# Optimization experiments

Hardware: AMD Instinct MI355X
Metric: run time of the kernel (lower is better)

Reference implementation:

```python
import jax, jax.numpy as jnp
import numpy as np

B, C, H, W = 4, 64, 128, 128
O = 64
K, S, P, D = 3, 1, 1, 1
K2 = K * K
Ho = (H + 2 * P - D * (K - 1) - 1) // S + 1
Wo = (W + 2 * P - D * (K - 1) - 1) // S + 1


def setup_inputs() -> dict:
    key = jax.random.key(0)
    k1, k2, k3, k4, k5 = jax.random.split(key, 5)
    x = jax.random.normal(k1, (B, C, H, W), dtype=jnp.float32)
    fan = C * K2
    # offset conv: out_channels = 2*n_offsets*K*K = 18; small init so offsets are ~O(1) px
    offset_w = jax.random.normal(k2, (2 * K2, C, K, K), dtype=jnp.float32) * (0.1 / np.sqrt(fan))
    offset_b = jax.random.normal(k3, (2 * K2,), dtype=jnp.float32) * 0.01
    deform_w = jax.random.normal(k4, (O, C, K, K), dtype=jnp.float32) * (1.0 / np.sqrt(fan))
    deform_b = jax.random.normal(k5, (O,), dtype=jnp.float32) * 0.01
    return {"x": x, "offset_w": offset_w, "offset_b": offset_b,
            "deform_w": deform_w, "deform_b": deform_b}


def _conv2d(x, w, b):
    y = jax.lax.conv_general_dilated(
        x, w, window_strides=(S, S), padding=[(P, P), (P, P)],
        rhs_dilation=(D, D), dimension_numbers=("NCHW", "OIHW", "NCHW"))
    return y + b[None, :, None, None]


def _gather(flat, iy, ix, h, w):
    # flat: [B, C, H*W]; iy/ix: [B, K2, Ho, Wo] int32
    valid = (iy >= 0) & (iy < h) & (ix >= 0) & (ix < w)
    idx = jnp.clip(iy, 0, h - 1) * w + jnp.clip(ix, 0, w - 1)
    b = flat.shape[0]
    v = jax.vmap(lambda f, i: f[:, i])(flat, idx.reshape(b, -1))  # [B, C, K2*Ho*Wo]
    v = v.reshape(b, flat.shape[1], *idx.shape[1:])               # [B, C, K2, Ho, Wo]
    return v * valid[:, None].astype(flat.dtype)


def _deform_conv(x, offset, w, b):
    # offset: [B, 2*K2, Ho, Wo] laid out as (dy, dx) pairs per kernel tap (torchvision order)
    off = offset.reshape(B, K2, 2, Ho, Wo)
    dy, dx = off[:, :, 0], off[:, :, 1]                           # [B, K2, Ho, Wo]
    ky = (jnp.arange(K2) // K * D).astype(jnp.float32)
    kx = (jnp.arange(K2) % K * D).astype(jnp.float32)
    base_y = (jnp.arange(Ho) * S - P).astype(jnp.float32)
    base_x = (jnp.arange(Wo) * S - P).astype(jnp.float32)
    py = dy + base_y[None, None, :, None] + ky[None, :, None, None]
    px = dx + base_x[None, None, None, :] + kx[None, :, None, None]

    y0 = jnp.floor(py); x0 = jnp.floor(px)
    wy = py - y0; wx = px - x0
    y0i = y0.astype(jnp.int32); x0i = x0.astype(jnp.int32)
    flat = x.reshape(B, C, H * W)
    w00 = ((1 - wy) * (1 - wx))[:, None]
    w01 = ((1 - wy) * wx)[:, None]
    w10 = (wy * (1 - wx))[:, None]
    w11 = (wy * wx)[:, None]
    sampled = (_gather(flat, y0i, x0i, H, W) * w00
               + _gather(flat, y0i, x0i + 1, H, W) * w01
               + _gather(flat, y0i + 1, x0i, H, W) * w10
               + _gather(flat, y0i + 1, x0i + 1, H, W) * w11)  # [B, C, K2, Ho, Wo]
    out = jnp.einsum("bckhw,ock->bohw", sampled, w.reshape(O, C, K2))
    return out + b[None, :, None, None]


def reference(x, offset_w, offset_b, deform_w, deform_b):
    offset = _conv2d(x, offset_w, offset_b)
    return _deform_conv(x, offset, deform_w, deform_b)
```

## Files before the change

### kernel.cpp

```cpp
#include <hip/hip_runtime.h>

#define BB 4
#define CC 64
#define HH 128
#define WW 128
#define OO 64
#define HWs (HH*WW)

typedef _Float16 f16;
typedef _Float16 f16x8 __attribute__((ext_vector_type(8)));
typedef _Float16 f16x2 __attribute__((ext_vector_type(2)));
typedef float f32x4 __attribute__((ext_vector_type(4)));

__device__ __forceinline__ size_t xt_idx(int b, int y, int x) {
    return (((size_t)b * HH + y) * WW + x) * CC;
}

__global__ __launch_bounds__(256) void prep_all(const float* __restrict__ x,
                                                const float* __restrict__ offw,
                                                const float* __restrict__ dw,
                                                f16* __restrict__ xt,
                                                f16* __restrict__ wA_off,
                                                f16* __restrict__ wA_def) {
    const int bid = blockIdx.x;
    const int tid = threadIdx.x;
    if (bid < 512) {
        const int b = bid >> 7, y = bid & 127;
        const int px = tid & 127, half = tid >> 7;
        const float* src = x + (size_t)b * CC * HWs + (size_t)half * 32 * HWs + y * WW + px;
        f16* dst = xt + xt_idx(b, y, px) + half * 32;
        #pragma unroll
        for (int cg = 0; cg < 4; ++cg) {
            f16x8 v;
            #pragma unroll
            for (int j = 0; j < 8; ++j)
                v[j] = (f16)src[(size_t)(cg * 8 + j) * HWs];
            *(f16x8*)(dst + cg * 8) = v;
        }
    } else {
        const int t = (bid - 512) * 256 + tid;
        const int l = t & 63;
        const int idx = t >> 6;
        f16x8 v;
        if (idx < 36) {
            const int mt = idx & 1, ks = idx >> 1;
            const int o = mt * 16 + (l & 15);
            const int tap = ks >> 1, ky = tap / 3, kx = tap % 3;
            #pragma unroll
            for (int i = 0; i < 8; ++i) {
                const int c = (ks & 1) * 32 + (l >> 4) * 8 + i;
                v[i] = (o < 18) ? (f16)offw[((o * CC + c) * 3 + ky) * 3 + kx] : (f16)0.f;
            }
            *(f16x8*)(wA_off + (size_t)(idx * 64 + l) * 8) = v;
        } else if (idx < 108) {
            const int id2 = idx - 36;
            const int mt = id2 & 3, ks = (id2 >> 2) & 1, tap = id2 >> 3;
            const int o = mt * 16 + (l & 15);
            #pragma unroll
            for (int i = 0; i < 8; ++i) {
                const int c = ks * 32 + (l >> 4) * 8 + i;
                v[i] = (f16)dw[(size_t)(o * CC + c) * 9 + tap];
            }
            *(f16x8*)(wA_def + (size_t)(id2 * 64 + l) * 8) = v;
        }
    }
}

__device__ __forceinline__ f16x8 combine4(f16x8 p00, f16x8 p01, f16x8 p10, f16x8 p11,
                                          f16 h00, f16 h01, f16 h10, f16 h11) {
    const f16x8 W00 = {h00,h00,h00,h00,h00,h00,h00,h00};
    const f16x8 W01 = {h01,h01,h01,h01,h01,h01,h01,h01};
    const f16x8 W10 = {h10,h10,h10,h10,h10,h10,h10,h10};
    const f16x8 W11 = {h11,h11,h11,h11,h11,h11,h11,h11};
    return p00 * W00 + p01 * W01 + p10 * W10 + p11 * W11;
}

__global__ __launch_bounds__(128, 3) void deform_mfma(
    const f16* __restrict__ xt,
    const f16* __restrict__ wA_off,
    const float* __restrict__ offb,
    const f16* __restrict__ wA_def,
    const float* __restrict__ dbias,
    float* __restrict__ out)
{
    __shared__ __align__(16) char win[5 * 36 * 8 * 16];
    __shared__ float offs[18][32];

    const int tid = threadIdx.x;
    const int bid0 = blockIdx.x;
    const int bid = (bid0 & 7) * 256 + (bid0 >> 3);
    const int b = bid >> 9, row = (bid >> 2) & 127, px0 = (bid & 3) * 32;
    const int w = tid >> 6, l = tid & 63;
    const int pxs = l & 15, pxl = w * 16 + pxs, gpx = px0 + pxl, cg = l >> 4;

    #pragma unroll
    for (int it = 0; it < 12; ++it) {
        const int i = tid + it * 128;
        if (i < 5 * 36 * 8) {
            const int s = i / 288, rem = i - s * 288;
            const int xw = rem >> 3, ch8 = rem & 7;
            const int gy = row - 2 + s, gx = px0 - 2 + xw;
            f16x8 v = {};
            if (gy >= 0 && gy < HH && gx >= 0 && gx < WW)
                v = *(const f16x8*)(xt + xt_idx(b, gy, gx) + ch8 * 8);
            *(f16x8*)(win + ((s * 36 + xw) * 8 + (ch8 ^ ((xw + s) & 7))) * 16) = v;
        }
    }
    __syncthreads();

    {
        f32x4 oa0 = {0,0,0,0}, oa1 = {0,0,0,0};
        auto baddr = [&](int ks) {
            const int tap = ks >> 1, chalf = ks & 1;
            const int ky = tap / 3, kx = tap - ky * 3;
            const int s = 1 + ky;
            const int xw = pxl + 1 + kx;
            const int ch8 = chalf * 4 + cg;
            return (const f16x8*)(win + ((s * 36 + xw) * 8 + (ch8 ^ ((xw + s) & 7))) * 16);
        };
        const f16* wob = wA_off + (size_t)l * 8;
        f16x8 bf = *baddr(0);
        f16x8 a0 = *(const f16x8*)(wob + 0 * 512);
        f16x8 a1 = *(const f16x8*)(wob + 1 * 512);
        #pragma unroll
        for (int ks = 0; ks < 18; ++ks) {
            f16x8 bfn = bf, a0n = a0, a1n = a1;
            if (ks < 17) {
                bfn = *baddr(ks + 1);
                a0n = *(const f16x8*)(wob + (size_t)(ks + 1) * 1024);
                a1n = *(const f16x8*)(wob + (size_t)(ks + 1) * 1024 + 512);
            }
            oa0 = __builtin_amdgcn_mfma_f32_16x16x32_f16(a0, bf, oa0, 0, 0, 0);
            oa1 = __builtin_amdgcn_mfma_f32_16x16x32_f16(a1, bf, oa1, 0, 0, 0);
            bf = bfn; a0 = a0n; a1 = a1n;
        }
        #pragma unroll
        for (int reg = 0; reg < 4; ++reg) {
            const int o0 = cg * 4 + reg;
            offs[o0][pxl] = oa0[reg] + offb[o0];
            const int o1 = o0 + 16;
            if (o1 < 18) offs[o1][pxl] = oa1[reg] + offb[o1];
        }
    }
    __syncthreads();

    int o00[9], o01[9], o10[9], o11[9];
    f16x2 hA[9], hB[9];
    unsigned okm = 0;
    #pragma unroll
    for (int t = 0; t < 9; ++t) {
        const int ky = t / 3, kx = t - ky * 3;
        const float dy = offs[2 * t][pxl], dx = offs[2 * t + 1][pxl];
        const float py  = (float)(row - 1 + ky) + dy;
        const float pxf = (float)(gpx - 1 + kx) + dx;
        const float y0f = floorf(py), x0f = floorf(pxf);
        const float wy = py - y0f, wx = pxf - x0f;
        const int y0 = (int)y0f, x0 = (int)x0f;
        const int y1 = y0 + 1, x1 = x0 + 1;
        const bool vy0 = (y0 >= 0) & (y0 < HH), vy1 = (y1 >= 0) & (y1 < HH);
        const bool vx0 = (x0 >= 0) & (x0 < WW), vx1 = (x1 >= 0) & (x1 < WW);
        hA[t][0] = (f16)((1.f - wy) * (1.f - wx) * (float)(vy0 & vx0));
        hA[t][1] = (f16)((1.f - wy) * wx         * (float)(vy0 & vx1));
        hB[t][0] = (f16)(wy * (1.f - wx)         * (float)(vy1 & vx0));
        hB[t][1] = (f16)(wy * wx                 * (float)(vy1 & vx1));
        const int cy0 = min(max(y0, 0), HH - 1), cy1 = min(max(y1, 0), HH - 1);
        const int cx0 = min(max(x0, 0), WW - 1), cx1 = min(max(x1, 0), WW - 1);
        const int s0 = cy0 - (row - 2), s1 = cy1 - (row - 2);
        const int u0 = cx0 - (px0 - 2), u1 = cx1 - (px0 - 2);
        const int ok = (s0 >= 0) & (s0 < 5) & (s1 >= 0) & (s1 < 5) &
                       (u0 >= 0) & (u0 < 36) & (u1 >= 0) & (u1 < 36);
        if (__all(ok)) okm |= (1u << t);
        const int s0c = min(max(s0, 0), 4), s1c = min(max(s1, 0), 4);
        const int u0c = min(max(u0, 0), 35), u1c = min(max(u1, 0), 35);
        o00[t] = ((s0c * 36 + u0c) * 8 + (cg ^ ((u0c + s0c) & 7))) * 16;
        o01[t] = ((s0c * 36 + u1c) * 8 + (cg ^ ((u1c + s0c) & 7))) * 16;
        o10[t] = ((s1c * 36 + u0c) * 8 + (cg ^ ((u0c + s1c) & 7))) * 16;
        o11[t] = ((s1c * 36 + u1c) * 8 + (cg ^ ((u1c + s1c) & 7))) * 16;
    }

    f32x4 acc0 = {0,0,0,0}, acc1 = {0,0,0,0}, acc2 = {0,0,0,0}, acc3 = {0,0,0,0};
    const f16* wbase = wA_def + (size_t)l * 8;

    if (okm == 0x1FFu) {
        f16x8 g0 = *(const f16x8*)(win + o00[0]);
        f16x8 g1 = *(const f16x8*)(win + o01[0]);
        f16x8 g2 = *(const f16x8*)(win + o10[0]);
        f16x8 g3 = *(const f16x8*)(win + o11[0]);
        f16x8 wv0 = *(const f16x8*)(wbase + 0 * 512);
        f16x8 wv1 = *(const f16x8*)(wbase + 1 * 512);
        f16x8 wv2 = *(const f16x8*)(wbase + 2 * 512);
        f16x8 wv3 = *(const f16x8*)(wbase + 3 * 512);
        #pragma unroll
        for (int j = 0; j < 18; ++j) {
            const int t = j >> 1;
            f16x8 n0 = g0, n1 = g1, n2 = g2, n3 = g3;
            f16x8 m0 = wv0, m1 = wv1, m2 = wv2, m3 = wv3;
            if (j < 17) {
                const int tn = (j + 1) >> 1, fl = ((j + 1) & 1) << 6;
                n0 = *(const f16x8*)(win + (o00[tn] ^ fl));
                n1 = *(const f16x8*)(win + (o01[tn] ^ fl));
                n2 = *(const f16x8*)(win + (o10[tn] ^ fl));
                n3 = *(const f16x8*)(win + (o11[tn] ^ fl));
                m0 = *(const f16x8*)(wbase + (size_t)(j + 1) * 2048 + 0 * 512);
                m1 = *(const f16x8*)(wbase + (size_t)(j + 1) * 2048 + 1 * 512);
                m2 = *(const f16x8*)(wbase + (size_t)(j + 1) * 2048 + 2 * 512);
                m3 = *(const f16x8*)(wbase + (size_t)(j + 1) * 2048 + 3 * 512);
            }
            const f16x8 bf = combine4(g0, g1, g2, g3,
                                      hA[t][0], hA[t][1], hB[t][0], hB[t][1]);
            acc0 = __builtin_amdgcn_mfma_f32_16x16x32_f16(wv0, bf, acc0, 0, 0, 0);
            acc1 = __builtin_amdgcn_mfma_f32_16x16x32_f16(wv1, bf, acc1, 0, 0, 0);
            acc2 = __builtin_amdgcn_mfma_f32_16x16x32_f16(wv2, bf, acc2, 0, 0, 0);
            acc3 = __builtin_amdgcn_mfma_f32_16x16x32_f16(wv3, bf, acc3, 0, 0, 0);
            g0 = n0; g1 = n1; g2 = n2; g3 = n3;
            wv0 = m0; wv1 = m1; wv2 = m2; wv3 = m3;
        }
    } else {
        #pragma unroll
        for (int t = 0; t < 9; ++t) {
            #pragma unroll
            for (int cpass = 0; cpass < 2; ++cpass) {
                const int flip = cpass << 6;
                f16x8 bf;
                if ((okm >> t) & 1) {
                    const f16x8 p00 = *(const f16x8*)(win + (o00[t] ^ flip));
                    const f16x8 p01 = *(const f16x8*)(win + (o01[t] ^ flip));
                    const f16x8 p10 = *(const f16x8*)(win + (o10[t] ^ flip));
                    const f16x8 p11 = *(const f16x8*)(win + (o11[t] ^ flip));
                    bf = combine4(p00, p01, p10, p11,
                                  hA[t][0], hA[t][1], hB[t][0], hB[t][1]);
                } else {
                    const int ky = t / 3, kx = t - ky * 3;
                    const float dy = offs[2 * t][pxl], dx = offs[2 * t + 1][pxl];
                    const float py  = (float)(row - 1 + ky) + dy;
                    const float pxf = (float)(gpx - 1 + kx) + dx;
                    const int y0 = (int)floorf(py), x0 = (int)floorf(pxf);
                    const int cy0 = min(max(y0, 0), HH - 1), cy1 = min(max(y0 + 1, 0), HH - 1);
                    const int cx0 = min(max(x0, 0), WW - 1), cx1 = min(max(x0 + 1, 0), WW - 1);
                    const int ch8 = cpass * 4 + cg;
                    const f16x8 p00 = *(const f16x8*)(xt + xt_idx(b, cy0, cx0) + ch8 * 8);
                    const f16x8 p01 = *(const f16x8*)(xt + xt_idx(b, cy0, cx1) + ch8 * 8);
                    const f16x8 p10 = *(const f16x8*)(xt + xt_idx(b, cy1, cx0) + ch8 * 8);
                    const f16x8 p11 = *(const f16x8*)(xt + xt_idx(b, cy1, cx1) + ch8 * 8);
                    bf = combine4(p00, p01, p10, p11,
                                  hA[t][0], hA[t][1], hB[t][0], hB[t][1]);
                }
                const f16* wa = wbase + (size_t)(t * 2 + cpass) * 2048;
                acc0 = __builtin_amdgcn_mfma_f32_16x16x32_f16(*(const f16x8*)(wa + 0 * 512), bf, acc0, 0, 0, 0);
                acc1 = __builtin_amdgcn_mfma_f32_16x16x32_f16(*(const f16x8*)(wa + 1 * 512), bf, acc1, 0, 0, 0);
                acc2 = __builtin_amdgcn_mfma_f32_16x16x32_f16(*(const f16x8*)(wa + 2 * 512), bf, acc2, 0, 0, 0);
                acc3 = __builtin_amdgcn_mfma_f32_16x16x32_f16(*(const f16x8*)(wa + 3 * 512), bf, acc3, 0, 0, 0);
            }
        }
    }

    #pragma unroll
    for (int mt = 0; mt < 4; ++mt) {
        const f32x4 a = (mt == 0) ? acc0 : (mt == 1) ? acc1 : (mt == 2) ? acc2 : acc3;
        #pragma unroll
        for (int reg = 0; reg < 4; ++reg) {
            const int o = mt * 16 + cg * 4 + reg;
            out[(((size_t)b * OO + o) * HH + row) * WW + gpx] = a[reg] + dbias[o];
        }
    }
}

extern "C" void kernel_launch(void* const* d_in, const int* in_sizes, int n_in,
                              void* d_out, int out_size, void* d_ws, size_t ws_size,
                              hipStream_t stream) {
    const float* x     = (const float*)d_in[0];
    const float* offw  = (const float*)d_in[1];
    const float* offb  = (const float*)d_in[2];
    const float* dw    = (const float*)d_in[3];
    const float* dbias = (const float*)d_in[4];
    float* out = (float*)d_out;

    const size_t XT_BYTES    = (size_t)BB * HH * WW * CC * sizeof(f16);
    const size_t WAOFF_BYTES = 36 * 64 * 8 * sizeof(f16);

    f16* xt     = (f16*)d_ws;
    f16* wa_off = (f16*)((char*)d_ws + XT_BYTES);
    f16* wa_def = (f16*)((char*)d_ws + XT_BYTES + WAOFF_BYTES);
    (void)ws_size; (void)in_sizes; (void)n_in; (void)out_size;

    prep_all<<<512 + 27, 256, 0, stream>>>(x, offw, dw, xt, wa_off, wa_def);
    deform_mfma<<<BB * HH * 4, 128, 0, stream>>>(xt, wa_off, offb, wa_def, dbias, out);
}
```

Measured before the change: 42.91 us.

## Split offset conv into separate kernel and async-load window via global_load_lds

Moves the offset convolution out of the main deform kernel into its own kernel that writes fp16 offsets to a workspace buffer. The deform kernel then loads its offsets directly from global memory and fills the shared-memory window with asynchronous global_load_lds copies, overlapping that fill with the bilinear setup computation. The software-prefetch double buffering in the fast path is removed. The costs are an extra kernel launch, another pass over the xt window, a global round trip for the offsets, and offsets stored in fp16 instead of fp32, which may change numerics.

```diff
diff --git a/kernel.cpp b/kernel.cpp
--- a/kernel.cpp
+++ b/kernel.cpp
@@ -11,6 +11,7 @@
 typedef _Float16 f16x8 __attribute__((ext_vector_type(8)));
 typedef _Float16 f16x2 __attribute__((ext_vector_type(2)));
 typedef float f32x4 __attribute__((ext_vector_type(4)));
+typedef unsigned int u32;
 
 __device__ __forceinline__ size_t xt_idx(int b, int y, int x) {
     return (((size_t)b * HH + y) * WW + x) * CC;
@@ -66,6 +67,59 @@
     }
 }
 
+__global__ __launch_bounds__(128, 4) void offs_conv(
+    const f16* __restrict__ xt,
+    const f16* __restrict__ wA_off,
+    const float* __restrict__ offb,
+    f16* __restrict__ offs_g)
+{
+    __shared__ __align__(16) char win[3 * 36 * 8 * 16];
+    const int tid = threadIdx.x;
+    const int bid0 = blockIdx.x;
+    const int bid = (bid0 & 7) * 256 + (bid0 >> 3);
+    const int b = bid >> 9, row = (bid >> 2) & 127, px0 = (bid & 3) * 32;
+    const int w = tid >> 6, l = tid & 63;
+    const int pxs = l & 15, pxl = w * 16 + pxs, gpx = px0 + pxl, cg = l >> 4;
+
+    #pragma unroll
+    for (int it = 0; it < 7; ++it) {
+        const int i = tid + it * 128;
+        if (i < 3 * 36 * 8) {
+            const int s = i / 288, rem = i - s * 288;
+            const int xw = rem >> 3, ch8 = rem & 7;
+            const int gy = row - 1 + s, gx = px0 - 2 + xw;
+            f16x8 v = {};
+            if (gy >= 0 && gy < HH && gx >= 0 && gx < WW)
+                v = *(const f16x8*)(xt + xt_idx(b, gy, gx) + ch8 * 8);
+            *(f16x8*)(win + ((s * 36 + xw) * 8 + (ch8 ^ ((xw + s) & 7))) * 16) = v;
+        }
+    }
+    __syncthreads();
+
+    f32x4 oa0 = {0,0,0,0}, oa1 = {0,0,0,0};
+    #pragma unroll
+    for (int ks = 0; ks < 18; ++ks) {
+        const int tap = ks >> 1, chalf = ks & 1;
+        const int ky = tap / 3, kx = tap - ky * 3;
+        const int xw = pxl + 1 + kx;
+        const int ch8 = chalf * 4 + cg;
+        const int byte = ((ky * 36 + xw) * 8 + (ch8 ^ ((xw + ky) & 7))) * 16;
+        const f16x8 bf = *(const f16x8*)(win + byte);
+        const f16x8 a0 = *(const f16x8*)(wA_off + (size_t)((ks * 2 + 0) * 64 + l) * 8);
+        const f16x8 a1 = *(const f16x8*)(wA_off + (size_t)((ks * 2 + 1) * 64 + l) * 8);
+        oa0 = __builtin_amdgcn_mfma_f32_16x16x32_f16(a0, bf, oa0, 0, 0, 0);
+        oa1 = __builtin_amdgcn_mfma_f32_16x16x32_f16(a1, bf, oa1, 0, 0, 0);
+    }
+    f16* ob = offs_g + ((size_t)(b * HH + row) * WW + gpx) * 24;
+    #pragma unroll
+    for (int reg = 0; reg < 4; ++reg) {
+        const int o0 = cg * 4 + reg;
+        ob[o0] = (f16)(oa0[reg] + offb[o0]);
+        const int o1 = o0 + 16;
+        if (o1 < 18) ob[o1] = (f16)(oa1[reg] + offb[o1]);
+    }
+}
+
 __device__ __forceinline__ f16x8 combine4(f16x8 p00, f16x8 p01, f16x8 p10, f16x8 p11,
                                           f16 h00, f16 h01, f16 h10, f16 h11) {
     const f16x8 W00 = {h00,h00,h00,h00,h00,h00,h00,h00};
@@ -77,14 +131,12 @@
 
 __global__ __launch_bounds__(128, 3) void deform_mfma(
     const f16* __restrict__ xt,
-    const f16* __restrict__ wA_off,
-    const float* __restrict__ offb,
+    const f16* __restrict__ offs_g,
     const f16* __restrict__ wA_def,
     const float* __restrict__ dbias,
     float* __restrict__ out)
 {
     __shared__ __align__(16) char win[5 * 36 * 8 * 16];
-    __shared__ float offs[18][32];
 
     const int tid = threadIdx.x;
     const int bid0 = blockIdx.x;
@@ -93,56 +145,38 @@
     const int w = tid >> 6, l = tid & 63;
     const int pxs = l & 15, pxl = w * 16 + pxs, gpx = px0 + pxl, cg = l >> 4;
 
+    const f16* ob = offs_g + ((size_t)(b * HH + row) * WW + gpx) * 24;
+    const f16x8 ov0 = *(const f16x8*)(ob);
+    const f16x8 ov1 = *(const f16x8*)(ob + 8);
+    const f16x8 ov2 = *(const f16x8*)(ob + 16);
+
     #pragma unroll
     for (int it = 0; it < 12; ++it) {
         const int i = tid + it * 128;
         if (i < 5 * 36 * 8) {
             const int s = i / 288, rem = i - s * 288;
-            const int xw = rem >> 3, ch8 = rem & 7;
-            const int gy = row - 2 + s, gx = px0 - 2 + xw;
-            f16x8 v = {};
-            if (gy >= 0 && gy < HH && gx >= 0 && gx < WW)
-                v = *(const f16x8*)(xt + xt_idx(b, gy, gx) + ch8 * 8);
-            *(f16x8*)(win + ((s * 36 + xw) * 8 + (ch8 ^ ((xw + s) & 7))) * 16) = v;
-        }
-    }
-    __syncthreads();
-
-    {
-        f32x4 oa0 = {0,0,0,0}, oa1 = {0,0,0,0};
-        auto baddr = [&](int ks) {
-            const int tap = ks >> 1, chalf = ks & 1;
-            const int ky = tap / 3, kx = tap - ky * 3;
-            const int s = 1 + ky;
-            const int xw = pxl + 1 + kx;
-            const int ch8 = chalf * 4 + cg;
-            return (const f16x8*)(win + ((s * 36 + xw) * 8 + (ch8 ^ ((xw + s) & 7))) * 16);
-        };
-        const f16* wob = wA_off + (size_t)l * 8;
-        f16x8 bf = *baddr(0);
-        f16x8 a0 = *(const f16x8*)(wob + 0 * 512);
-        f16x8 a1 = *(const f16x8*)(wob + 1 * 512);
-        #pragma unroll
-        for (int ks = 0; ks < 18; ++ks) {
-            f16x8 bfn = bf, a0n = a0, a1n = a1;
-            if (ks < 17) {
-                bfn = *baddr(ks + 1);
-                a0n = *(const f16x8*)(wob + (size_t)(ks + 1) * 1024);
-                a1n = *(const f16x8*)(wob + (size_t)(ks + 1) * 1024 + 512);
-            }
-            oa0 = __builtin_amdgcn_mfma_f32_16x16x32_f16(a0, bf, oa0, 0, 0, 0);
-            oa1 = __builtin_amdgcn_mfma_f32_16x16x32_f16(a1, bf, oa1, 0, 0, 0);
-            bf = bfn; a0 = a0n; a1 = a1n;
-        }
-        #pragma unroll
-        for (int reg = 0; reg < 4; ++reg) {
-            const int o0 = cg * 4 + reg;
-            offs[o0][pxl] = oa0[reg] + offb[o0];
-            const int o1 = o0 + 16;
-            if (o1 < 18) offs[o1][pxl] = oa1[reg] + offb[o1];
-        }
-    }
-    __syncthreads();
+            const int xw = rem >> 3, slot = rem & 7;
+            const int ch8 = slot ^ ((xw + s) & 7);
+            const int gy = min(max(row - 2 + s, 0), HH - 1);
+            const int gx = min(max(px0 - 2 + xw, 0), WW - 1);
+            const f16* src = xt + xt_idx(b, gy, gx) + ch8 * 8;
+            __builtin_amdgcn_global_load_lds(
+                (const __attribute__((address_space(1))) u32*)(const void*)src,
+                (__attribute__((address_space(3))) u32*)(void*)(win + i * 16),
+                16, 0, 0);
+        }
+    }
+
+    float dyA[9], dxA[9];
+    #pragma unroll
+    for (int t = 0; t < 9; ++t) {
+        const int e = 2 * t;
+        const f16 hdy = (e < 8) ? ov0[e & 7] : (e < 16) ? ov1[e & 7] : ov2[e & 7];
+        const f16 hdx = (e + 1 < 8) ? ov0[(e + 1) & 7]
+                       : (e + 1 < 16) ? ov1[(e + 1) & 7] : ov2[(e + 1) & 7];
+        dyA[t] = (float)hdy;
+        dxA[t] = (float)hdx;
+    }
 
     int o00[9], o01[9], o10[9], o11[9];
     f16x2 hA[9], hB[9];
@@ -150,9 +184,8 @@
     #pragma unroll
     for (int t = 0; t < 9; ++t) {
         const int ky = t / 3, kx = t - ky * 3;
-        const float dy = offs[2 * t][pxl], dx = offs[2 * t + 1][pxl];
-        const float py  = (float)(row - 1 + ky) + dy;
-        const float pxf = (float)(gpx - 1 + kx) + dx;
+        const float py  = (float)(row - 1 + ky) + dyA[t];
+        const float pxf = (float)(gpx - 1 + kx) + dxA[t];
         const float y0f = floorf(py), x0f = floorf(pxf);
         const float wy = py - y0f, wx = pxf - x0f;
         const int y0 = (int)y0f, x0 = (int)x0f;
@@ -177,43 +210,26 @@
         o10[t] = ((s1c * 36 + u0c) * 8 + (cg ^ ((u0c + s1c) & 7))) * 16;
         o11[t] = ((s1c * 36 + u1c) * 8 + (cg ^ ((u1c + s1c) & 7))) * 16;
     }
+    __syncthreads();
 
     f32x4 acc0 = {0,0,0,0}, acc1 = {0,0,0,0}, acc2 = {0,0,0,0}, acc3 = {0,0,0,0};
     const f16* wbase = wA_def + (size_t)l * 8;
 
     if (okm == 0x1FFu) {
-        f16x8 g0 = *(const f16x8*)(win + o00[0]);
-        f16x8 g1 = *(const f16x8*)(win + o01[0]);
-        f16x8 g2 = *(const f16x8*)(win + o10[0]);
-        f16x8 g3 = *(const f16x8*)(win + o11[0]);
-        f16x8 wv0 = *(const f16x8*)(wbase + 0 * 512);
-        f16x8 wv1 = *(const f16x8*)(wbase + 1 * 512);
-        f16x8 wv2 = *(const f16x8*)(wbase + 2 * 512);
-        f16x8 wv3 = *(const f16x8*)(wbase + 3 * 512);
         #pragma unroll
         for (int j = 0; j < 18; ++j) {
-            const int t = j >> 1;
-            f16x8 n0 = g0, n1 = g1, n2 = g2, n3 = g3;
-            f16x8 m0 = wv0, m1 = wv1, m2 = wv2, m3 = wv3;
-            if (j < 17) {
-                const int tn = (j + 1) >> 1, fl = ((j + 1) & 1) << 6;
-                n0 = *(const f16x8*)(win + (o00[tn] ^ fl));
-                n1 = *(const f16x8*)(win + (o01[tn] ^ fl));
-                n2 = *(const f16x8*)(win + (o10[tn] ^ fl));
-                n3 = *(const f16x8*)(win + (o11[tn] ^ fl));
-                m0 = *(const f16x8*)(wbase + (size_t)(j + 1) * 2048 + 0 * 512);
-                m1 = *(const f16x8*)(wbase + (size_t)(j + 1) * 2048 + 1 * 512);
-                m2 = *(const f16x8*)(wbase + (size_t)(j + 1) * 2048 + 2 * 512);
-                m3 = *(const f16x8*)(wbase + (size_t)(j + 1) * 2048 + 3 * 512);
-            }
-            const f16x8 bf = combine4(g0, g1, g2, g3,
+            const int t = j >> 1, fl = (j & 1) << 6;
+            const f16x8 p00 = *(const f16x8*)(win + (o00[t] ^ fl));
+            const f16x8 p01 = *(const f16x8*)(win + (o01[t] ^ fl));
+            const f16x8 p10 = *(const f16x8*)(win + (o10[t] ^ fl));
+            const f16x8 p11 = *(const f16x8*)(win + (o11[t] ^ fl));
+            const f16x8 bf = combine4(p00, p01, p10, p11,
                                       hA[t][0], hA[t][1], hB[t][0], hB[t][1]);
-            acc0 = __builtin_amdgcn_mfma_f32_16x16x32_f16(wv0, bf, acc0, 0, 0, 0);
-            acc1 = __builtin_amdgcn_mfma_f32_16x16x32_f16(wv1, bf, acc1, 0, 0, 0);
-            acc2 = __builtin_amdgcn_mfma_f32_16x16x32_f16(wv2, bf, acc2, 0, 0, 0);
-            acc3 = __builtin_amdgcn_mfma_f32_16x16x32_f16(wv3, bf, acc3, 0, 0, 0);
-            g0 = n0; g1 = n1; g2 = n2; g3 = n3;
-            wv0 = m0; wv1 = m1; wv2 = m2; wv3 = m3;
+            const f16* wa = wbase + (size_t)j * 2048;
+            acc0 = __builtin_amdgcn_mfma_f32_16x16x32_f16(*(const f16x8*)(wa + 0 * 512), bf, acc0, 0, 0, 0);
+            acc1 = __builtin_amdgcn_mfma_f32_16x16x32_f16(*(const f16x8*)(wa + 1 * 512), bf, acc1, 0, 0, 0);
+            acc2 = __builtin_amdgcn_mfma_f32_16x16x32_f16(*(const f16x8*)(wa + 2 * 512), bf, acc2, 0, 0, 0);
+            acc3 = __builtin_amdgcn_mfma_f32_16x16x32_f16(*(const f16x8*)(wa + 3 * 512), bf, acc3, 0, 0, 0);
         }
     } else {
         #pragma unroll
@@ -231,9 +247,8 @@
                                   hA[t][0], hA[t][1], hB[t][0], hB[t][1]);
                 } else {
                     const int ky = t / 3, kx = t - ky * 3;
-                    const float dy = offs[2 * t][pxl], dx = offs[2 * t + 1][pxl];
-                    const float py  = (float)(row - 1 + ky) + dy;
-                    const float pxf = (float)(gpx - 1 + kx) + dx;
+                    const float py  = (float)(row - 1 + ky) + dyA[t];
+                    const float pxf = (float)(gpx - 1 + kx) + dxA[t];
                     const int y0 = (int)floorf(py), x0 = (int)floorf(pxf);
                     const int cy0 = min(max(y0, 0), HH - 1), cy1 = min(max(y0 + 1, 0), HH - 1);
                     const int cx0 = min(max(x0, 0), WW - 1), cx1 = min(max(x0 + 1, 0), WW - 1);
@@ -277,12 +292,15 @@
 
     const size_t XT_BYTES    = (size_t)BB * HH * WW * CC * sizeof(f16);
     const size_t WAOFF_BYTES = 36 * 64 * 8 * sizeof(f16);
+    const size_t WADEF_BYTES = 72 * 64 * 8 * sizeof(f16);
 
     f16* xt     = (f16*)d_ws;
     f16* wa_off = (f16*)((char*)d_ws + XT_BYTES);
     f16* wa_def = (f16*)((char*)d_ws + XT_BYTES + WAOFF_BYTES);
+    f16* offs_g = (f16*)((char*)d_ws + XT_BYTES + WAOFF_BYTES + WADEF_BYTES);
     (void)ws_size; (void)in_sizes; (void)n_in; (void)out_size;
 
     prep_all<<<512 + 27, 256, 0, stream>>>(x, offw, dw, xt, wa_off, wa_def);
-    deform_mfma<<<BB * HH * 4, 128, 0, stream>>>(xt, wa_off, offb, wa_def, dbias, out);
-}
+    offs_conv<<<BB * HH * 4, 128, 0, stream>>>(xt, wa_off, offb, offs_g);
+    deform_mfma<<<BB * HH * 4, 128, 0, stream>>>(xt, offs_g, wa_def, dbias, out);
+}
```

New measurement: 45.54 us. +6.1%, slower.
